# Optimization experiments

Hardware: AMD Instinct MI355X
Metric: run time of the kernel (lower is better)

## Reference

```python
import jax, jax.numpy as jnp
import numpy as np

K_NN = 3  # pointnet2 relation default k=3


def setup_inputs() -> dict:
    key = jax.random.key(0)
    k1, k2, k3 = jax.random.split(key, 3)
    B, N, S, C = 4, 16384, 4096, 256
    q = jax.random.normal(k1, (B, N, 3), dtype=jnp.float32)
    k = jax.random.normal(k2, (B, S, 3), dtype=jnp.float32)
    v = jax.random.normal(k3, (B, S, C), dtype=jnp.float32)
    return {"q": q, "k": k, "v": v}


def reference(q, k, v):
    # squared pairwise distance: ||q||^2 - 2 q.k + ||k||^2  -> [B, N, S]
    d = (
        jnp.sum(q * q, axis=-1, keepdims=True)
        - 2.0 * jnp.einsum("bnd,bsd->bns", q, k)
        + jnp.sum(k * k, axis=-1)[:, None, :]
    )
    # 3 nearest neighbors (smallest distances)
    neg_d, idx = jax.lax.top_k(-d, K_NN)          # [B, N, 3]
    dists = -neg_d
    recip = 1.0 / (dists + 1e-8)
    weight = recip / jnp.sum(recip, axis=-1, keepdims=True)  # [B, N, 3]
    # score is zero except at idx; scatter+dense matmul == gather-weighted sum
    B = q.shape[0]
    vg = v[jnp.arange(B)[:, None, None], idx]     # [B, N, 3, C]
    extract = jnp.einsum("bnk,bnkc->bnc", weight, vg)  # [B, N, C]
    return jnp.transpose(extract, (0, 2, 1))      # [B, C, N] (embed is identity)
```

## Files before the change

### kernel.cpp

```cpp
#include <hip/hip_runtime.h>

#define BB 4
#define NN 16384
#define SS 4096
#define CC 256
#define SEG 1024
#define RQ 4
#define TLD 132

typedef float f32x4 __attribute__((ext_vector_type(4)));

__device__ __forceinline__ bool lexlt(float da, int ia, float db, int ib) {
  return (da < db) || ((da == db) && (ia < ib));
}

__global__ __launch_bounds__(256, 8) void scan_kernel(
    const float* __restrict__ qg, const float* __restrict__ kg,
    float4* __restrict__ dpart, int4* __restrict__ ipart) {
#pragma clang fp contract(off)
  __shared__ __align__(16) float4 kpts[SEG];
  float* md = (float*)kpts;
  int* mi = (int*)((char*)kpts + 6144);

  const int tid = threadIdx.x;
  const int blk = blockIdx.x;
  const int b = blk >> 9;
  const int seg = (blk >> 7) & 3;
  const int n0 = (blk & 127) << 7;
  const int qlane = tid & 31;
  const int g = tid >> 5;

  float qx[RQ], qy[RQ], qz[RQ], qq[RQ];
  float d0[RQ], d1[RQ], d2[RQ];
  int i0[RQ], i1[RQ], i2[RQ];
#pragma unroll
  for (int j = 0; j < RQ; ++j) {
    int n = n0 + qlane + 32 * j;
    const float* qp = qg + ((long)b * NN + n) * 3;
    qx[j] = qp[0]; qy[j] = qp[1]; qz[j] = qp[2];
    qq[j] = (qx[j] * qx[j] + qy[j] * qy[j]) + qz[j] * qz[j];
    d0[j] = 3.4e38f; d1[j] = 3.4e38f; d2[j] = 3.4e38f;
    i0[j] = 0; i1[j] = 0; i2[j] = 0;
  }

  {
    const float* kb = kg + ((long)b * SS + (long)seg * SEG) * 3;
    const float4* src = (const float4*)kb + tid * 3;
    float4 f0 = src[0], f1 = src[1], f2 = src[2];
    float px[4] = {f0.x, f0.w, f1.z, f2.y};
    float py[4] = {f0.y, f1.x, f1.w, f2.z};
    float pz[4] = {f0.z, f1.y, f2.x, f2.w};
#pragma unroll
    for (int m = 0; m < 4; ++m) {
      float kk = (px[m] * px[m] + py[m] * py[m]) + pz[m] * pz[m];
      kpts[tid * 4 + m] = make_float4(px[m], py[m], pz[m], kk);
    }
  }
  __syncthreads();

  const int sbase = seg * SEG + g * 128;
#pragma unroll 2
  for (int i = 0; i < 128; ++i) {
    float4 kp = kpts[g * 128 + i];
    const int s = sbase + i;
#pragma unroll
    for (int j = 0; j < RQ; ++j) {
      float dot = (qx[j] * kp.x + qy[j] * kp.y) + qz[j] * kp.z;
      float d = __builtin_fmaf(dot, -2.0f, qq[j]) + kp.w;
      bool k2 = d < d2[j];
      bool k1 = d < d1[j];
      bool k0 = d < d0[j];
      float nd2 = __builtin_amdgcn_fmed3f(d, d1[j], d2[j]);
      float nd1 = __builtin_amdgcn_fmed3f(d, d0[j], d1[j]);
      float nd0 = fminf(d, d0[j]);
      i2[j] = k1 ? i1[j] : (k2 ? s : i2[j]);
      i1[j] = k0 ? i0[j] : (k1 ? s : i1[j]);
      i0[j] = k0 ? s : i0[j];
      d2[j] = nd2; d1[j] = nd1; d0[j] = nd0;
    }
  }

#pragma unroll
  for (int j = 0; j < RQ; ++j) {
    float E0 = __shfl_xor(d0[j], 32), E1 = __shfl_xor(d1[j], 32), E2 = __shfl_xor(d2[j], 32);
    int F0 = __shfl_xor(i0[j], 32), F1 = __shfl_xor(i1[j], 32), F2 = __shfl_xor(i2[j], 32);
    float A0 = d0[j], A1 = d1[j], A2 = d2[j];
    int B0 = i0[j], B1 = i1[j], B2 = i2[j];
    bool t = lexlt(E0, F0, A0, B0);
    float r0 = t ? E0 : A0; int s0 = t ? F0 : B0;
    float nA0 = t ? A0 : A1, nA1 = t ? A1 : A2;
    int nB0 = t ? B0 : B1, nB1 = t ? B1 : B2;
    float nE0 = t ? E1 : E0, nE1 = t ? E2 : E1;
    int nF0 = t ? F1 : F0, nF1 = t ? F2 : F1;
    bool u = lexlt(nE0, nF0, nA0, nB0);
    float r1 = u ? nE0 : nA0; int s1 = u ? nF0 : nB0;
    float mA0 = u ? nA0 : nA1; int mB0 = u ? nB0 : nB1;
    float mE0 = u ? nE1 : nE0; int mF0 = u ? nF1 : nF0;
    bool w = lexlt(mE0, mF0, mA0, mB0);
    float r2 = w ? mE0 : mA0; int s2 = w ? mF0 : mB0;
    d0[j] = r0; d1[j] = r1; d2[j] = r2;
    i0[j] = s0; i1[j] = s1; i2[j] = s2;
  }

  __syncthreads();
  if ((tid & 63) < 32) {
    const int wv = tid >> 6;
#pragma unroll
    for (int j = 0; j < RQ; ++j) {
      int base = (((wv * 32) + qlane) * RQ + j) * 3;
      md[base + 0] = d0[j]; md[base + 1] = d1[j]; md[base + 2] = d2[j];
      mi[base + 0] = i0[j]; mi[base + 1] = i1[j]; mi[base + 2] = i2[j];
    }
  }
  __syncthreads();

  if (tid < 128) {
    const int qi = tid;
    const int ql = qi & 31, jj = qi >> 5;
    float D0 = 3.4e38f, D1 = 3.4e38f, D2 = 3.4e38f;
    int I0 = -1, I1 = -1, I2 = -1;
    for (int wv = 0; wv < 4; ++wv) {
      int base = ((wv * 32 + ql) * RQ + jj) * 3;
      for (int r = 0; r < 3; ++r) {
        float d = md[base + r];
        int s = mi[base + r];
        if (lexlt(d, s, D2, I2)) {
          if (lexlt(d, s, D1, I1)) {
            D2 = D1; I2 = I1;
            if (lexlt(d, s, D0, I0)) { D1 = D0; I1 = I0; D0 = d; I0 = s; }
            else { D1 = d; I1 = s; }
          } else { D2 = d; I2 = s; }
        }
      }
    }
    long gid = (long)b * NN + n0 + qi;
    dpart[gid * 4 + seg] = make_float4(D0, D1, D2, 0.0f);
    ipart[gid * 4 + seg] = make_int4(I0, I1, I2, 0);
  }
}

__global__ __launch_bounds__(256, 4) void gather_kernel(
    const float* __restrict__ vg, const float4* __restrict__ dpart,
    const int4* __restrict__ ipart, float* __restrict__ outg) {
#pragma clang fp contract(off)
  __shared__ __align__(16) float tile[64 * TLD];
  __shared__ float sw[64][3];
  __shared__ int si[64][3];

  const int tid = threadIdx.x;
  const int bid = blockIdx.x;
  const int xcd = bid & 7;
  const int b = xcd >> 1;
  const int chunk = xcd & 1;
  const int nblk = bid >> 3;
  const int n0 = nblk << 6;

  if (tid < 64) {
    long gid = (long)b * NN + n0 + tid;
    float D0 = 3.4e38f, D1 = 3.4e38f, D2 = 3.4e38f;
    int I0 = -1, I1 = -1, I2 = -1;
#pragma unroll
    for (int seg = 0; seg < 4; ++seg) {
      float4 dv = dpart[gid * 4 + seg];
      int4 iv = ipart[gid * 4 + seg];
      float ds_[3] = {dv.x, dv.y, dv.z};
      int is_[3] = {iv.x, iv.y, iv.z};
      for (int r = 0; r < 3; ++r) {
        float d = ds_[r];
        int s = is_[r];
        if (lexlt(d, s, D2, I2)) {
          if (lexlt(d, s, D1, I1)) {
            D2 = D1; I2 = I1;
            if (lexlt(d, s, D0, I0)) { D1 = D0; I1 = I0; D0 = d; I0 = s; }
            else { D1 = d; I1 = s; }
          } else { D2 = d; I2 = s; }
        }
      }
    }
    float r0 = 1.0f / (D0 + 1e-8f);
    float r1 = 1.0f / (D1 + 1e-8f);
    float r2 = 1.0f / (D2 + 1e-8f);
    float rs = (r0 + r1) + r2;
    sw[tid][0] = r0 / rs; sw[tid][1] = r1 / rs; sw[tid][2] = r2 / rs;
    si[tid][0] = I0; si[tid][1] = I1; si[tid][2] = I2;
  }
  __syncthreads();

  const int wv = tid >> 6;
  const int lane = tid & 63;
  const int qh = lane >> 5;
  const int slot = lane & 31;
  const float* vb = vg + (long)b * SS * CC + chunk * 128;

#pragma unroll 4
  for (int it = 0; it < 8; ++it) {
    int qs = wv * 16 + it * 2 + qh;
    float w0 = sw[qs][0], w1 = sw[qs][1], w2 = sw[qs][2];
    const float4* r0p = (const float4*)(vb + (long)si[qs][0] * CC);
    const float4* r1p = (const float4*)(vb + (long)si[qs][1] * CC);
    const float4* r2p = (const float4*)(vb + (long)si[qs][2] * CC);
    float4 a0 = r0p[slot], a1 = r1p[slot], a2 = r2p[slot];
    float4 acc;
    acc.x = (w0 * a0.x + w1 * a1.x) + w2 * a2.x;
    acc.y = (w0 * a0.y + w1 * a1.y) + w2 * a2.y;
    acc.z = (w0 * a0.z + w1 * a1.z) + w2 * a2.z;
    acc.w = (w0 * a0.w + w1 * a1.w) + w2 * a2.w;
    *(float4*)&tile[qs * TLD + slot * 4] = acc;
  }
  __syncthreads();

  {
    const int nf = tid & 15;
    const int cb0 = tid >> 4;
    const int q0 = nf << 2;
#pragma unroll 2
    for (int it = 0; it < 8; ++it) {
      int cl = cb0 + it * 16;
      int cch = (chunk << 7) + cl;
      f32x4 val;
      val.x = tile[(q0 + 0) * TLD + cl];
      val.y = tile[(q0 + 1) * TLD + cl];
      val.z = tile[(q0 + 2) * TLD + cl];
      val.w = tile[(q0 + 3) * TLD + cl];
      __builtin_nontemporal_store(
          val, (f32x4*)&outg[((long)(b * CC + cch)) * NN + n0 + q0]);
    }
  }
}

extern "C" void kernel_launch(void* const* d_in, const int* in_sizes, int n_in,
                              void* d_out, int out_size, void* d_ws, size_t ws_size,
                              hipStream_t stream) {
  const float* q = (const float*)d_in[0];
  const float* k = (const float*)d_in[1];
  const float* v = (const float*)d_in[2];
  float* out = (float*)d_out;
  float4* dpart = (float4*)d_ws;
  int4* ipart = (int4*)((char*)d_ws + (size_t)BB * NN * 4 * 16);
  hipLaunchKernelGGL(scan_kernel, dim3(2048), dim3(256), 0, stream, q, k, dpart, ipart);
  hipLaunchKernelGGL(gather_kernel, dim3(2048), dim3(256), 0, stream, v, dpart, ipart, out);
}
```

Baseline: 227.1 us.

## Fuse kNN scan and weighted gather into a single kernel

Merges the scan and gather kernels into one kernel in which each block scans all four key segments for 64 queries (RQ=2) and then gathers and writes both channel chunks. This drops the global round trip for the partial top-3 results and one kernel launch. It also adds an XOR swizzle on the shared-memory transpose tile to reduce bank conflicts. In exchange, per-thread work in the scan drops (RQ 4 to 2, so less reuse of each loaded key), the grid shrinks to 1024 blocks, and occupancy is lower at launch bounds 4.

```diff
diff --git a/kernel.cpp b/kernel.cpp
--- a/kernel.cpp
+++ b/kernel.cpp
@@ -4,8 +4,7 @@
 #define NN 16384
 #define SS 4096
 #define CC 256
-#define SEG 1024
-#define RQ 4
+#define RQ 2
 #define TLD 132
 
 typedef float f32x4 __attribute__((ext_vector_type(4)));
@@ -14,19 +13,24 @@
   return (da < db) || ((da == db) && (ia < ib));
 }
 
-__global__ __launch_bounds__(256, 8) void scan_kernel(
+__global__ __launch_bounds__(256, 4) void fused_kernel(
     const float* __restrict__ qg, const float* __restrict__ kg,
-    float4* __restrict__ dpart, int4* __restrict__ ipart) {
+    const float* __restrict__ vg, float* __restrict__ outg) {
 #pragma clang fp contract(off)
-  __shared__ __align__(16) float4 kpts[SEG];
-  float* md = (float*)kpts;
-  int* mi = (int*)((char*)kpts + 6144);
+  __shared__ __align__(16) char buf[64 * TLD * 4];
+  __shared__ float sw[64][3];
+  __shared__ int si[64][3];
+  float4* kpts = (float4*)buf;
+  float* tile = (float*)buf;
+  float* md = (float*)buf;
+  int* mi = (int*)(buf + 3072);
 
   const int tid = threadIdx.x;
-  const int blk = blockIdx.x;
-  const int b = blk >> 9;
-  const int seg = (blk >> 7) & 3;
-  const int n0 = (blk & 127) << 7;
+  const int bid = blockIdx.x;
+  const int b = (bid >> 1) & 3;
+  const int nh = bid & 1;
+  const int nblk = bid >> 3;
+  const int n0 = (nh * 128 + nblk) << 6;
   const int qlane = tid & 31;
   const int g = tid >> 5;
 
@@ -43,41 +47,44 @@
     i0[j] = 0; i1[j] = 0; i2[j] = 0;
   }
 
-  {
-    const float* kb = kg + ((long)b * SS + (long)seg * SEG) * 3;
-    const float4* src = (const float4*)kb + tid * 3;
-    float4 f0 = src[0], f1 = src[1], f2 = src[2];
-    float px[4] = {f0.x, f0.w, f1.z, f2.y};
-    float py[4] = {f0.y, f1.x, f1.w, f2.z};
-    float pz[4] = {f0.z, f1.y, f2.x, f2.w};
-#pragma unroll
-    for (int m = 0; m < 4; ++m) {
-      float kk = (px[m] * px[m] + py[m] * py[m]) + pz[m] * pz[m];
-      kpts[tid * 4 + m] = make_float4(px[m], py[m], pz[m], kk);
-    }
-  }
-  __syncthreads();
-
-  const int sbase = seg * SEG + g * 128;
+  for (int r = 0; r < 4; ++r) {
+    {
+      const float* kb = kg + ((long)b * SS + (long)r * 1024) * 3;
+      const float4* src = (const float4*)kb + tid * 3;
+      float4 f0 = src[0], f1 = src[1], f2 = src[2];
+      float px[4] = {f0.x, f0.w, f1.z, f2.y};
+      float py[4] = {f0.y, f1.x, f1.w, f2.z};
+      float pz[4] = {f0.z, f1.y, f2.x, f2.w};
+#pragma unroll
+      for (int m = 0; m < 4; ++m) {
+        float kk = (px[m] * px[m] + py[m] * py[m]) + pz[m] * pz[m];
+        kpts[tid * 4 + m] = make_float4(px[m], py[m], pz[m], kk);
+      }
+    }
+    __syncthreads();
+
+    const int sbase = r * 1024 + g * 128;
 #pragma unroll 2
-  for (int i = 0; i < 128; ++i) {
-    float4 kp = kpts[g * 128 + i];
-    const int s = sbase + i;
-#pragma unroll
-    for (int j = 0; j < RQ; ++j) {
-      float dot = (qx[j] * kp.x + qy[j] * kp.y) + qz[j] * kp.z;
-      float d = __builtin_fmaf(dot, -2.0f, qq[j]) + kp.w;
-      bool k2 = d < d2[j];
-      bool k1 = d < d1[j];
-      bool k0 = d < d0[j];
-      float nd2 = __builtin_amdgcn_fmed3f(d, d1[j], d2[j]);
-      float nd1 = __builtin_amdgcn_fmed3f(d, d0[j], d1[j]);
-      float nd0 = fminf(d, d0[j]);
-      i2[j] = k1 ? i1[j] : (k2 ? s : i2[j]);
-      i1[j] = k0 ? i0[j] : (k1 ? s : i1[j]);
-      i0[j] = k0 ? s : i0[j];
-      d2[j] = nd2; d1[j] = nd1; d0[j] = nd0;
-    }
+    for (int i = 0; i < 128; ++i) {
+      float4 kp = kpts[g * 128 + i];
+      const int s = sbase + i;
+#pragma unroll
+      for (int j = 0; j < RQ; ++j) {
+        float dot = (qx[j] * kp.x + qy[j] * kp.y) + qz[j] * kp.z;
+        float d = __builtin_fmaf(dot, -2.0f, qq[j]) + kp.w;
+        bool k2 = d < d2[j];
+        bool k1 = d < d1[j];
+        bool k0 = d < d0[j];
+        float nd2 = __builtin_amdgcn_fmed3f(d, d1[j], d2[j]);
+        float nd1 = __builtin_amdgcn_fmed3f(d, d0[j], d1[j]);
+        float nd0 = fminf(d, d0[j]);
+        i2[j] = k1 ? i1[j] : (k2 ? s : i2[j]);
+        i1[j] = k0 ? i0[j] : (k1 ? s : i1[j]);
+        i0[j] = k0 ? s : i0[j];
+        d2[j] = nd2; d1[j] = nd1; d0[j] = nd0;
+      }
+    }
+    __syncthreads();
   }
 
 #pragma unroll
@@ -102,7 +109,6 @@
     i0[j] = s0; i1[j] = s1; i2[j] = s2;
   }
 
-  __syncthreads();
   if ((tid & 63) < 32) {
     const int wv = tid >> 6;
 #pragma unroll
@@ -114,9 +120,8 @@
   }
   __syncthreads();
 
-  if (tid < 128) {
-    const int qi = tid;
-    const int ql = qi & 31, jj = qi >> 5;
+  if (tid < 64) {
+    const int ql = tid & 31, jj = tid >> 5;
     float D0 = 3.4e38f, D1 = 3.4e38f, D2 = 3.4e38f;
     int I0 = -1, I1 = -1, I2 = -1;
     for (int wv = 0; wv < 4; ++wv) {
@@ -133,50 +138,6 @@
         }
       }
     }
-    long gid = (long)b * NN + n0 + qi;
-    dpart[gid * 4 + seg] = make_float4(D0, D1, D2, 0.0f);
-    ipart[gid * 4 + seg] = make_int4(I0, I1, I2, 0);
-  }
-}
-
-__global__ __launch_bounds__(256, 4) void gather_kernel(
-    const float* __restrict__ vg, const float4* __restrict__ dpart,
-    const int4* __restrict__ ipart, float* __restrict__ outg) {
-#pragma clang fp contract(off)
-  __shared__ __align__(16) float tile[64 * TLD];
-  __shared__ float sw[64][3];
-  __shared__ int si[64][3];
-
-  const int tid = threadIdx.x;
-  const int bid = blockIdx.x;
-  const int xcd = bid & 7;
-  const int b = xcd >> 1;
-  const int chunk = xcd & 1;
-  const int nblk = bid >> 3;
-  const int n0 = nblk << 6;
-
-  if (tid < 64) {
-    long gid = (long)b * NN + n0 + tid;
-    float D0 = 3.4e38f, D1 = 3.4e38f, D2 = 3.4e38f;
-    int I0 = -1, I1 = -1, I2 = -1;
-#pragma unroll
-    for (int seg = 0; seg < 4; ++seg) {
-      float4 dv = dpart[gid * 4 + seg];
-      int4 iv = ipart[gid * 4 + seg];
-      float ds_[3] = {dv.x, dv.y, dv.z};
-      int is_[3] = {iv.x, iv.y, iv.z};
-      for (int r = 0; r < 3; ++r) {
-        float d = ds_[r];
-        int s = is_[r];
-        if (lexlt(d, s, D2, I2)) {
-          if (lexlt(d, s, D1, I1)) {
-            D2 = D1; I2 = I1;
-            if (lexlt(d, s, D0, I0)) { D1 = D0; I1 = I0; D0 = d; I0 = s; }
-            else { D1 = d; I1 = s; }
-          } else { D2 = d; I2 = s; }
-        }
-      }
-    }
     float r0 = 1.0f / (D0 + 1e-8f);
     float r1 = 1.0f / (D1 + 1e-8f);
     float r2 = 1.0f / (D2 + 1e-8f);
@@ -186,45 +147,50 @@
   }
   __syncthreads();
 
-  const int wv = tid >> 6;
+  const int wv4 = tid >> 6;
   const int lane = tid & 63;
   const int qh = lane >> 5;
   const int slot = lane & 31;
-  const float* vb = vg + (long)b * SS * CC + chunk * 128;
-
+  const int nf = tid & 15;
+  const int cb0 = tid >> 4;
+
+#pragma unroll
+  for (int chunk = 0; chunk < 2; ++chunk) {
+    const float* vb = vg + (long)b * SS * CC + (chunk << 7);
 #pragma unroll 4
-  for (int it = 0; it < 8; ++it) {
-    int qs = wv * 16 + it * 2 + qh;
-    float w0 = sw[qs][0], w1 = sw[qs][1], w2 = sw[qs][2];
-    const float4* r0p = (const float4*)(vb + (long)si[qs][0] * CC);
-    const float4* r1p = (const float4*)(vb + (long)si[qs][1] * CC);
-    const float4* r2p = (const float4*)(vb + (long)si[qs][2] * CC);
-    float4 a0 = r0p[slot], a1 = r1p[slot], a2 = r2p[slot];
-    float4 acc;
-    acc.x = (w0 * a0.x + w1 * a1.x) + w2 * a2.x;
-    acc.y = (w0 * a0.y + w1 * a1.y) + w2 * a2.y;
-    acc.z = (w0 * a0.z + w1 * a1.z) + w2 * a2.z;
-    acc.w = (w0 * a0.w + w1 * a1.w) + w2 * a2.w;
-    *(float4*)&tile[qs * TLD + slot * 4] = acc;
-  }
-  __syncthreads();
-
-  {
-    const int nf = tid & 15;
-    const int cb0 = tid >> 4;
-    const int q0 = nf << 2;
+    for (int it = 0; it < 8; ++it) {
+      int qs = wv4 * 16 + it * 2 + qh;
+      float w0 = sw[qs][0], w1 = sw[qs][1], w2 = sw[qs][2];
+      const float4* r0p = (const float4*)(vb + (long)si[qs][0] * CC);
+      const float4* r1p = (const float4*)(vb + (long)si[qs][1] * CC);
+      const float4* r2p = (const float4*)(vb + (long)si[qs][2] * CC);
+      float4 a0 = r0p[slot], a1 = r1p[slot], a2 = r2p[slot];
+      float4 acc;
+      acc.x = (w0 * a0.x + w1 * a1.x) + w2 * a2.x;
+      acc.y = (w0 * a0.y + w1 * a1.y) + w2 * a2.y;
+      acc.z = (w0 * a0.z + w1 * a1.z) + w2 * a2.z;
+      acc.w = (w0 * a0.w + w1 * a1.w) + w2 * a2.w;
+      int col = (slot ^ ((qs >> 2) & 7)) << 2;
+      *(float4*)&tile[qs * TLD + col] = acc;
+    }
+    __syncthreads();
+    {
+      const int q0 = nf << 2;
 #pragma unroll 2
-    for (int it = 0; it < 8; ++it) {
-      int cl = cb0 + it * 16;
-      int cch = (chunk << 7) + cl;
-      f32x4 val;
-      val.x = tile[(q0 + 0) * TLD + cl];
-      val.y = tile[(q0 + 1) * TLD + cl];
-      val.z = tile[(q0 + 2) * TLD + cl];
-      val.w = tile[(q0 + 3) * TLD + cl];
-      __builtin_nontemporal_store(
-          val, (f32x4*)&outg[((long)(b * CC + cch)) * NN + n0 + q0]);
-    }
+      for (int it = 0; it < 8; ++it) {
+        int cl = cb0 + it * 16;
+        int cch = (chunk << 7) + cl;
+        int colw = (((cl >> 2) ^ (nf & 7)) << 2) | (cl & 3);
+        f32x4 val;
+        val.x = tile[(q0 + 0) * TLD + colw];
+        val.y = tile[(q0 + 1) * TLD + colw];
+        val.z = tile[(q0 + 2) * TLD + colw];
+        val.w = tile[(q0 + 3) * TLD + colw];
+        __builtin_nontemporal_store(
+            val, (f32x4*)&outg[((long)(b * CC + cch)) * NN + n0 + q0]);
+      }
+    }
+    __syncthreads();
   }
 }
 
@@ -235,8 +201,5 @@
   const float* k = (const float*)d_in[1];
   const float* v = (const float*)d_in[2];
   float* out = (float*)d_out;
-  float4* dpart = (float4*)d_ws;
-  int4* ipart = (int4*)((char*)d_ws + (size_t)BB * NN * 4 * 16);
-  hipLaunchKernelGGL(scan_kernel, dim3(2048), dim3(256), 0, stream, q, k, dpart, ipart);
-  hipLaunchKernelGGL(gather_kernel, dim3(2048), dim3(256), 0, stream, v, dpart, ipart, out);
+  hipLaunchKernelGGL(fused_kernel, dim3(1024), dim3(256), 0, stream, q, k, v, out);
 }
```

New measurement: 241.5 us. +6.3%, slower.

## Restructure scan to one query per thread with wave-level early rejection

Applied to the files above, without the earlier changes.

The scan kernel now assigns one query per thread over the whole 1024-point segment. This replaces the earlier scheme of 4 queries per thread with split segments, a shuffle merge and a shared-memory merge. After the first 256 candidates it uses the current third-best distance as a threshold and skips the top-3 insertion logic whenever no lane in the wave beats it. The aim is to cut the per-candidate select/compare ALU work and remove the merge overhead. In exchange, each thread does four times more serial iterations, the grid is halved, and the skip test adds wave divergence and ballot cost.

```diff
diff --git a/kernel.cpp b/kernel.cpp
--- a/kernel.cpp
+++ b/kernel.cpp
@@ -4,8 +4,6 @@
 #define NN 16384
 #define SS 4096
 #define CC 256
-#define SEG 1024
-#define RQ 4
 #define TLD 132
 
 typedef float f32x4 __attribute__((ext_vector_type(4)));
@@ -14,37 +12,23 @@
   return (da < db) || ((da == db) && (ia < ib));
 }
 
-__global__ __launch_bounds__(256, 8) void scan_kernel(
+__global__ __launch_bounds__(256, 4) void scan_kernel(
     const float* __restrict__ qg, const float* __restrict__ kg,
     float4* __restrict__ dpart, int4* __restrict__ ipart) {
 #pragma clang fp contract(off)
-  __shared__ __align__(16) float4 kpts[SEG];
-  float* md = (float*)kpts;
-  int* mi = (int*)((char*)kpts + 6144);
+  __shared__ __align__(16) float4 kpts[1024];
 
   const int tid = threadIdx.x;
   const int blk = blockIdx.x;
-  const int b = blk >> 9;
-  const int seg = (blk >> 7) & 3;
-  const int n0 = (blk & 127) << 7;
-  const int qlane = tid & 31;
-  const int g = tid >> 5;
-
-  float qx[RQ], qy[RQ], qz[RQ], qq[RQ];
-  float d0[RQ], d1[RQ], d2[RQ];
-  int i0[RQ], i1[RQ], i2[RQ];
-#pragma unroll
-  for (int j = 0; j < RQ; ++j) {
-    int n = n0 + qlane + 32 * j;
-    const float* qp = qg + ((long)b * NN + n) * 3;
-    qx[j] = qp[0]; qy[j] = qp[1]; qz[j] = qp[2];
-    qq[j] = (qx[j] * qx[j] + qy[j] * qy[j]) + qz[j] * qz[j];
-    d0[j] = 3.4e38f; d1[j] = 3.4e38f; d2[j] = 3.4e38f;
-    i0[j] = 0; i1[j] = 0; i2[j] = 0;
-  }
+  const int b = blk >> 8;
+  const int seg = (blk >> 6) & 3;
+  const int n0 = (blk & 63) << 8;
+  const int wv = tid >> 6;
+  const int lane = tid & 63;
+  const int q = n0 + wv * 64 + lane;
 
   {
-    const float* kb = kg + ((long)b * SS + (long)seg * SEG) * 3;
+    const float* kb = kg + ((long)b * SS + (long)seg * 1024) * 3;
     const float4* src = (const float4*)kb + tid * 3;
     float4 f0 = src[0], f1 = src[1], f2 = src[2];
     float px[4] = {f0.x, f0.w, f1.z, f2.y};
@@ -56,87 +40,61 @@
       kpts[tid * 4 + m] = make_float4(px[m], py[m], pz[m], kk);
     }
   }
+
+  const float* qp = qg + ((long)b * NN + q) * 3;
+  float qx = qp[0], qy = qp[1], qz = qp[2];
+  float qq = (qx * qx + qy * qy) + qz * qz;
+  float d0 = 3.4e38f, d1 = 3.4e38f, d2 = 3.4e38f;
+  int i0 = 0, i1 = 0, i2 = 0;
   __syncthreads();
 
-  const int sbase = seg * SEG + g * 128;
-#pragma unroll 2
-  for (int i = 0; i < 128; ++i) {
-    float4 kp = kpts[g * 128 + i];
-    const int s = sbase + i;
-#pragma unroll
-    for (int j = 0; j < RQ; ++j) {
-      float dot = (qx[j] * kp.x + qy[j] * kp.y) + qz[j] * kp.z;
-      float d = __builtin_fmaf(dot, -2.0f, qq[j]) + kp.w;
-      bool k2 = d < d2[j];
-      bool k1 = d < d1[j];
-      bool k0 = d < d0[j];
-      float nd2 = __builtin_amdgcn_fmed3f(d, d1[j], d2[j]);
-      float nd1 = __builtin_amdgcn_fmed3f(d, d0[j], d1[j]);
-      float nd0 = fminf(d, d0[j]);
-      i2[j] = k1 ? i1[j] : (k2 ? s : i2[j]);
-      i1[j] = k0 ? i0[j] : (k1 ? s : i1[j]);
-      i0[j] = k0 ? s : i0[j];
-      d2[j] = nd2; d1[j] = nd1; d0[j] = nd0;
-    }
-  }
-
-#pragma unroll
-  for (int j = 0; j < RQ; ++j) {
-    float E0 = __shfl_xor(d0[j], 32), E1 = __shfl_xor(d1[j], 32), E2 = __shfl_xor(d2[j], 32);
-    int F0 = __shfl_xor(i0[j], 32), F1 = __shfl_xor(i1[j], 32), F2 = __shfl_xor(i2[j], 32);
-    float A0 = d0[j], A1 = d1[j], A2 = d2[j];
-    int B0 = i0[j], B1 = i1[j], B2 = i2[j];
-    bool t = lexlt(E0, F0, A0, B0);
-    float r0 = t ? E0 : A0; int s0 = t ? F0 : B0;
-    float nA0 = t ? A0 : A1, nA1 = t ? A1 : A2;
-    int nB0 = t ? B0 : B1, nB1 = t ? B1 : B2;
-    float nE0 = t ? E1 : E0, nE1 = t ? E2 : E1;
-    int nF0 = t ? F1 : F0, nF1 = t ? F2 : F1;
-    bool u = lexlt(nE0, nF0, nA0, nB0);
-    float r1 = u ? nE0 : nA0; int s1 = u ? nF0 : nB0;
-    float mA0 = u ? nA0 : nA1; int mB0 = u ? nB0 : nB1;
-    float mE0 = u ? nE1 : nE0; int mF0 = u ? nF1 : nF0;
-    bool w = lexlt(mE0, mF0, mA0, mB0);
-    float r2 = w ? mE0 : mA0; int s2 = w ? mF0 : mB0;
-    d0[j] = r0; d1[j] = r1; d2[j] = r2;
-    i0[j] = s0; i1[j] = s1; i2[j] = s2;
-  }
-
-  __syncthreads();
-  if ((tid & 63) < 32) {
-    const int wv = tid >> 6;
-#pragma unroll
-    for (int j = 0; j < RQ; ++j) {
-      int base = (((wv * 32) + qlane) * RQ + j) * 3;
-      md[base + 0] = d0[j]; md[base + 1] = d1[j]; md[base + 2] = d2[j];
-      mi[base + 0] = i0[j]; mi[base + 1] = i1[j]; mi[base + 2] = i2[j];
-    }
-  }
-  __syncthreads();
-
-  if (tid < 128) {
-    const int qi = tid;
-    const int ql = qi & 31, jj = qi >> 5;
-    float D0 = 3.4e38f, D1 = 3.4e38f, D2 = 3.4e38f;
-    int I0 = -1, I1 = -1, I2 = -1;
-    for (int wv = 0; wv < 4; ++wv) {
-      int base = ((wv * 32 + ql) * RQ + jj) * 3;
-      for (int r = 0; r < 3; ++r) {
-        float d = md[base + r];
-        int s = mi[base + r];
-        if (lexlt(d, s, D2, I2)) {
-          if (lexlt(d, s, D1, I1)) {
-            D2 = D1; I2 = I1;
-            if (lexlt(d, s, D0, I0)) { D1 = D0; I1 = I0; D0 = d; I0 = s; }
-            else { D1 = d; I1 = s; }
-          } else { D2 = d; I2 = s; }
-        }
+  const int sb = seg * 1024;
+
+#pragma unroll 4
+  for (int i = 0; i < 256; ++i) {
+    float4 kp = kpts[i];
+    float dot = (qx * kp.x + qy * kp.y) + qz * kp.z;
+    float d = __builtin_fmaf(dot, -2.0f, qq) + kp.w;
+    const int s = sb + i;
+    bool k2 = d < d2;
+    bool k1 = d < d1;
+    bool k0 = d < d0;
+    float nd2 = __builtin_amdgcn_fmed3f(d, d1, d2);
+    float nd1 = __builtin_amdgcn_fmed3f(d, d0, d1);
+    float nd0 = fminf(d, d0);
+    i2 = k1 ? i1 : (k2 ? s : i2);
+    i1 = k0 ? i0 : (k1 ? s : i1);
+    i0 = k0 ? s : i0;
+    d2 = nd2; d1 = nd1; d0 = nd0;
+  }
+
+  for (int c = 1; c < 4; ++c) {
+    const float tau = d2;
+    const int base = c * 256;
+#pragma unroll 4
+    for (int i = 0; i < 256; ++i) {
+      float4 kp = kpts[base + i];
+      float dot = (qx * kp.x + qy * kp.y) + qz * kp.z;
+      float d = __builtin_fmaf(dot, -2.0f, qq) + kp.w;
+      if (__builtin_expect(__any(d < tau), 0)) {
+        const int s = sb + base + i;
+        bool k2 = d < d2;
+        bool k1 = d < d1;
+        bool k0 = d < d0;
+        float nd2 = __builtin_amdgcn_fmed3f(d, d1, d2);
+        float nd1 = __builtin_amdgcn_fmed3f(d, d0, d1);
+        float nd0 = fminf(d, d0);
+        i2 = k1 ? i1 : (k2 ? s : i2);
+        i1 = k0 ? i0 : (k1 ? s : i1);
+        i0 = k0 ? s : i0;
+        d2 = nd2; d1 = nd1; d0 = nd0;
       }
     }
-    long gid = (long)b * NN + n0 + qi;
-    dpart[gid * 4 + seg] = make_float4(D0, D1, D2, 0.0f);
-    ipart[gid * 4 + seg] = make_int4(I0, I1, I2, 0);
-  }
+  }
+
+  long gid = (long)b * NN + q;
+  dpart[gid * 4 + seg] = make_float4(d0, d1, d2, 0.0f);
+  ipart[gid * 4 + seg] = make_int4(i0, i1, i2, 0);
 }
 
 __global__ __launch_bounds__(256, 4) void gather_kernel(
@@ -237,6 +195,6 @@
   float* out = (float*)d_out;
   float4* dpart = (float4*)d_ws;
   int4* ipart = (int4*)((char*)d_ws + (size_t)BB * NN * 4 * 16);
-  hipLaunchKernelGGL(scan_kernel, dim3(2048), dim3(256), 0, stream, q, k, dpart, ipart);
+  hipLaunchKernelGGL(scan_kernel, dim3(1024), dim3(256), 0, stream, q, k, dpart, ipart);
   hipLaunchKernelGGL(gather_kernel, dim3(2048), dim3(256), 0, stream, v, dpart, ipart, out);
 }
```

New measurement: 219.7 us. 1.03x faster.

## Gate later segment scans with a threshold from the first segment's top-3

Applied to the files above, without the earlier changes.

The nearest-neighbour scan becomes two kernels. The first computes the exact top-3 over key segment 0. The second scans segments 1–3 with one query per thread and skips the top-3 insertion logic whenever no lane in the wave has a distance at or below a threshold. That threshold is the smaller of segment 0's third-best distance and the running third-best. This removes most of the compare/select/med3 insertion work, but it adds a wave-wide vote and branch per key point, an extra kernel launch, and more LDS reads per query because each thread now covers one query instead of four.

```diff
diff --git a/kernel.cpp b/kernel.cpp
--- a/kernel.cpp
+++ b/kernel.cpp
@@ -3,9 +3,8 @@
 #define BB 4
 #define NN 16384
 #define SS 4096
+#define RQ 4
 #define CC 256
-#define SEG 1024
-#define RQ 4
 #define TLD 132
 
 typedef float f32x4 __attribute__((ext_vector_type(4)));
@@ -14,18 +13,17 @@
   return (da < db) || ((da == db) && (ia < ib));
 }
 
-__global__ __launch_bounds__(256, 8) void scan_kernel(
+__global__ __launch_bounds__(256, 8) void scan0_kernel(
     const float* __restrict__ qg, const float* __restrict__ kg,
     float4* __restrict__ dpart, int4* __restrict__ ipart) {
 #pragma clang fp contract(off)
-  __shared__ __align__(16) float4 kpts[SEG];
+  __shared__ __align__(16) float4 kpts[1024];
   float* md = (float*)kpts;
   int* mi = (int*)((char*)kpts + 6144);
 
   const int tid = threadIdx.x;
   const int blk = blockIdx.x;
-  const int b = blk >> 9;
-  const int seg = (blk >> 7) & 3;
+  const int b = blk >> 7;
   const int n0 = (blk & 127) << 7;
   const int qlane = tid & 31;
   const int g = tid >> 5;
@@ -44,7 +42,7 @@
   }
 
   {
-    const float* kb = kg + ((long)b * SS + (long)seg * SEG) * 3;
+    const float* kb = kg + (long)b * SS * 3;
     const float4* src = (const float4*)kb + tid * 3;
     float4 f0 = src[0], f1 = src[1], f2 = src[2];
     float px[4] = {f0.x, f0.w, f1.z, f2.y};
@@ -58,7 +56,7 @@
   }
   __syncthreads();
 
-  const int sbase = seg * SEG + g * 128;
+  const int sbase = g * 128;
 #pragma unroll 2
   for (int i = 0; i < 128; ++i) {
     float4 kp = kpts[g * 128 + i];
@@ -134,9 +132,78 @@
       }
     }
     long gid = (long)b * NN + n0 + qi;
-    dpart[gid * 4 + seg] = make_float4(D0, D1, D2, 0.0f);
-    ipart[gid * 4 + seg] = make_int4(I0, I1, I2, 0);
-  }
+    dpart[gid * 4 + 0] = make_float4(D0, D1, D2, 0.0f);
+    ipart[gid * 4 + 0] = make_int4(I0, I1, I2, 0);
+  }
+}
+
+__global__ __launch_bounds__(256, 4) void scan_gated_kernel(
+    const float* __restrict__ qg, const float* __restrict__ kg,
+    float4* __restrict__ dpart, int4* __restrict__ ipart) {
+#pragma clang fp contract(off)
+  __shared__ __align__(16) float4 kpts[1024];
+
+  const int tid = threadIdx.x;
+  const int blk = blockIdx.x;
+  const int b = blk / 192;
+  const int r_ = blk - b * 192;
+  const int seg = 1 + (r_ >> 6);
+  const int n0 = (r_ & 63) << 8;
+  const int wv = tid >> 6;
+  const int lane = tid & 63;
+  const int q = n0 + wv * 64 + lane;
+
+  {
+    const float* kb = kg + ((long)b * SS + (long)seg * 1024) * 3;
+    const float4* src = (const float4*)kb + tid * 3;
+    float4 f0 = src[0], f1 = src[1], f2 = src[2];
+    float px[4] = {f0.x, f0.w, f1.z, f2.y};
+    float py[4] = {f0.y, f1.x, f1.w, f2.z};
+    float pz[4] = {f0.z, f1.y, f2.x, f2.w};
+#pragma unroll
+    for (int m = 0; m < 4; ++m) {
+      float kk = (px[m] * px[m] + py[m] * py[m]) + pz[m] * pz[m];
+      kpts[tid * 4 + m] = make_float4(px[m], py[m], pz[m], kk);
+    }
+  }
+
+  const long gid = (long)b * NN + q;
+  const float* qp = qg + gid * 3;
+  float qx = qp[0], qy = qp[1], qz = qp[2];
+  float qq = (qx * qx + qy * qy) + qz * qz;
+  const float taub = dpart[gid * 4 + 0].z;
+  float d0 = 3.4e38f, d1 = 3.4e38f, d2 = 3.4e38f;
+  int i0 = 0, i1 = 0, i2 = 0;
+  __syncthreads();
+
+  const int sb = seg * 1024;
+
+  for (int c = 0; c < 4; ++c) {
+    const float tau = fminf(taub, d2);
+    const int base = c * 256;
+#pragma unroll 4
+    for (int i = 0; i < 256; ++i) {
+      float4 kp = kpts[base + i];
+      float dot = (qx * kp.x + qy * kp.y) + qz * kp.z;
+      float d = __builtin_fmaf(dot, -2.0f, qq) + kp.w;
+      if (__builtin_expect(__any(d <= tau), 0)) {
+        const int s = sb + base + i;
+        bool k2 = d < d2;
+        bool k1 = d < d1;
+        bool k0 = d < d0;
+        float nd2 = __builtin_amdgcn_fmed3f(d, d1, d2);
+        float nd1 = __builtin_amdgcn_fmed3f(d, d0, d1);
+        float nd0 = fminf(d, d0);
+        i2 = k1 ? i1 : (k2 ? s : i2);
+        i1 = k0 ? i0 : (k1 ? s : i1);
+        i0 = k0 ? s : i0;
+        d2 = nd2; d1 = nd1; d0 = nd0;
+      }
+    }
+  }
+
+  dpart[gid * 4 + seg] = make_float4(d0, d1, d2, 0.0f);
+  ipart[gid * 4 + seg] = make_int4(i0, i1, i2, 0);
 }
 
 __global__ __launch_bounds__(256, 4) void gather_kernel(
@@ -237,6 +304,7 @@
   float* out = (float*)d_out;
   float4* dpart = (float4*)d_ws;
   int4* ipart = (int4*)((char*)d_ws + (size_t)BB * NN * 4 * 16);
-  hipLaunchKernelGGL(scan_kernel, dim3(2048), dim3(256), 0, stream, q, k, dpart, ipart);
+  hipLaunchKernelGGL(scan0_kernel, dim3(512), dim3(256), 0, stream, q, k, dpart, ipart);
+  hipLaunchKernelGGL(scan_gated_kernel, dim3(768), dim3(256), 0, stream, q, k, dpart, ipart);
   hipLaunchKernelGGL(gather_kernel, dim3(2048), dim3(256), 0, stream, v, dpart, ipart, out);
 }
```

Result: slower. 238.4 us (+5.0%).
